# Performance work log

Measured on AMD Instinct MI355X. Metric: run time of the kernel, lower is better.

The kernel has to match this reference:

```python
import jax, jax.numpy as jnp
import numpy as np

RNN_NUM = 4  # rnn_num mean-field iterations


def setup_inputs() -> dict:
    key = jax.random.key(0)
    k1, k2, k3, k4 = jax.random.split(key, 4)
    T, N, M, K = 16384, 256, 8, 16  # time steps, regions, features, gaussian kernels
    inputs = jax.random.normal(k1, (T, N, M), dtype=jnp.float32)
    kernels = jax.random.uniform(k2, (N, N, K), dtype=jnp.float32)  # positive -> stable denominator
    W_feat = jax.random.uniform(k3, (1, M), dtype=jnp.float32) * 0.01  # feature_linear_layer.weight (F_in[1]=1, F_in[0]=M)
    W_lin = jax.random.uniform(k4, (1, K), dtype=jnp.float32) * 0.01   # linear_layer.weight (1, D_in)
    return {"inputs": inputs, "kernels": kernels, "W_feat": W_feat, "W_lin": W_lin}


def reference(inputs, kernels, W_feat, W_lin):
    # inputs: (T, N, M); kernels: (N, N, K); W_feat: (1, M); W_lin: (1, K)
    x = inputs @ W_feat.T                 # feature_layer -> (T, N, 1)
    originals = x
    # feature_layer(ones(T,N,M)) is constant: every entry equals sum(W_feat)
    f_weights = jnp.sum(W_feat)           # scalar, broadcasts as (T, N, 1)
    # static_conv_layer(all_ones, kernels): conv1d with length-1 input of ones
    # == row-sum of each kernel slice -> (N, K); loop-invariant, compute once.
    ones_conv = kernels.sum(axis=1)       # (N, K)
    denom = f_weights + 2.0 * (ones_conv @ W_lin.T)  # (N, 1), broadcasts over T
    for _ in range(RNN_NUM):
        # static_conv_layer(x, kernels): conv1d(length=1) == matmul per kernel slice,
        # fused over all K slices: out[t,i,k] = sum_j x[t,j] * kernels[i,j,k]
        conv = jnp.einsum('tj,ijk->tik', x[:, :, 0], kernels)  # (T, N, K)
        numer = originals + 2.0 * (conv @ W_lin.T)             # (T, N, 1)
        x = numer / denom
    return x
```

## Files before the change

kernel.cpp:

```cpp
#include <hip/hip_runtime.h>


#define NREG 256
#define KG   16
#define MF   8

typedef unsigned short u16;
typedef __attribute__((ext_vector_type(8))) short short8;
typedef __attribute__((ext_vector_type(4))) float f32x4;

__device__ __forceinline__ void async_copy16(const void* g, void* l) {
    __builtin_amdgcn_global_load_lds(
        (const __attribute__((address_space(1))) void*)g,
        (__attribute__((address_space(3))) void*)l,
        16, 0, 0);
}

__device__ __forceinline__ f32x4 ld16(const float* p) {
    f32x4 d;
    asm volatile("global_load_dwordx4 %0, %1, off" : "=v"(d) : "v"(p));
    return d;
}

__device__ __forceinline__ u16 bf16_rne(float x) {
    unsigned u = __float_as_uint(x);
    return (u16)((u + 0x7FFFu + ((u >> 16) & 1u)) >> 16);
}
__device__ __forceinline__ float bf16_to_f(u16 h) {
    return __uint_as_float(((unsigned)h) << 16);
}

__global__ __launch_bounds__(256) void k_prep(const float* __restrict__ kern,
                                              const float* __restrict__ Wlin,
                                              const float* __restrict__ Wfeat,
                                              float* __restrict__ B,
                                              float* __restrict__ Einv) {
    const int i = blockIdx.x, j = threadIdx.x;
    const float* kp = kern + ((size_t)i * NREG + j) * KG;
    float4 w0 = *(const float4*)(Wlin + 0);
    float4 w1 = *(const float4*)(Wlin + 4);
    float4 w2 = *(const float4*)(Wlin + 8);
    float4 w3 = *(const float4*)(Wlin + 12);
    float4 v0 = *(const float4*)(kp + 0);
    float4 v1 = *(const float4*)(kp + 4);
    float4 v2 = *(const float4*)(kp + 8);
    float4 v3 = *(const float4*)(kp + 12);
    float km = v0.x*w0.x + v0.y*w0.y + v0.z*w0.z + v0.w*w0.w
             + v1.x*w1.x + v1.y*w1.y + v1.z*w1.z + v1.w*w1.w
             + v2.x*w2.x + v2.y*w2.y + v2.z*w2.z + v2.w*w2.w
             + v3.x*w3.x + v3.y*w3.y + v3.z*w3.z + v3.w*w3.w;

    __shared__ float red[256];
    red[j] = km;
    __syncthreads();
    for (int s = 128; s > 0; s >>= 1) {
        if (j < s) red[j] += red[j + s];
        __syncthreads();
    }
    __shared__ float sden;
    if (j == 0) {
        float fw = 0.f;
#pragma unroll
        for (int m = 0; m < MF; ++m) fw += Wfeat[m];
        float den = fw + 2.f * red[0];
        sden = den;
        Einv[i] = 1.f / den;
    }
    __syncthreads();
    B[(size_t)i * NREG + j] = 2.f * km / sden;
}

#define MM1_BODY(Ar, Bm, acc)                                                 \
    _Pragma("unroll 4")                                                       \
    for (int l = 0; l < NREG; l += 8) {                                       \
        float b0 = Bm[(size_t)(l + 0) * NREG + tid];                          \
        float b1 = Bm[(size_t)(l + 1) * NREG + tid];                          \
        float b2 = Bm[(size_t)(l + 2) * NREG + tid];                          \
        float b3 = Bm[(size_t)(l + 3) * NREG + tid];                          \
        float b4 = Bm[(size_t)(l + 4) * NREG + tid];                          \
        float b5 = Bm[(size_t)(l + 5) * NREG + tid];                          \
        float b6 = Bm[(size_t)(l + 6) * NREG + tid];                          \
        float b7 = Bm[(size_t)(l + 7) * NREG + tid];                          \
        acc += Ar[l+0]*b0 + Ar[l+1]*b1 + Ar[l+2]*b2 + Ar[l+3]*b3              \
             + Ar[l+4]*b4 + Ar[l+5]*b5 + Ar[l+6]*b6 + Ar[l+7]*b7;             \
    }

__global__ __launch_bounds__(256) void k_mm(const float* __restrict__ A,
                                            const float* __restrict__ Bm,
                                            float* __restrict__ Out) {
    const int tid = threadIdx.x;
    const int i = blockIdx.x;
    __shared__ float Ar[NREG];
    Ar[tid] = A[(size_t)i * NREG + tid];
    __syncthreads();
    float acc = 0.f;
    MM1_BODY(Ar, Bm, acc)
    Out[(size_t)i * NREG + tid] = acc;
}

__global__ __launch_bounds__(256) void k_mm2comb(const float* __restrict__ B,
                                                 const float* __restrict__ C,
                                                 const float* __restrict__ Einv,
                                                 u16* __restrict__ Mh,
                                                 u16* __restrict__ Ml) {
    const int tid = threadIdx.x;
    const int i = blockIdx.x;
    __shared__ float Ar[NREG];

    Ar[tid] = B[(size_t)i * NREG + tid];
    __syncthreads();
    float g1 = 0.f;
    MM1_BODY(Ar, C, g1)
    __syncthreads();
    Ar[tid] = C[(size_t)i * NREG + tid];
    __syncthreads();
    float g2 = 0.f;
    MM1_BODY(Ar, C, g2)

    const size_t idx = (size_t)i * NREG + tid;
    float v = ((i == tid) ? 1.f : 0.f) + B[idx] + C[idx] + g1;
    v = v * Einv[tid] + g2;
    u16 h = bf16_rne(v);
    Mh[idx] = h;
    Ml[idx] = bf16_rne(v - bf16_to_f(h));
}

__global__ __launch_bounds__(512, 1) void k_main(const float* __restrict__ in,
                                                 const float* __restrict__ Wfeat,
                                                 const u16* __restrict__ Mh,
                                                 const u16* __restrict__ Ml,
                                                 float* __restrict__ out) {
    __shared__ __align__(16) u16 Ah[64 * 256];
    __shared__ __align__(16) u16 Al[64 * 256];
    __shared__ __align__(16) u16 Bh[256 * 64];
    __shared__ __align__(16) u16 Bl[256 * 64];

    const int tid = threadIdx.x, lane = tid & 63, wid = tid >> 6;
    const size_t t0 = (size_t)blockIdx.x * 64;

    float4 wa = *(const float4*)(Wfeat);
    float4 wb = *(const float4*)(Wfeat + 4);
    asm volatile("" :: "v"(wa.x), "v"(wa.y), "v"(wa.z), "v"(wa.w),
                       "v"(wb.x), "v"(wb.y), "v"(wb.z), "v"(wb.w));

    const float* rowbase = in + (t0 + wid * 8) * (NREG * MF);

#define ISSUE(BUF, TL)                                                        \
    {                                                                         \
        const float* rp_ = rowbase + (TL) * 2048 + lane * 8;                  \
        _Pragma("unroll")                                                     \
        for (int q = 0; q < 8; ++q)                                           \
            BUF[q] = ld16(rp_ + (q >> 1) * 512 + (q & 1) * 4);                \
    }

#define PROCESS(BUF, TL)                                                      \
    {                                                                         \
        const int t_ = wid * 8 + (TL);                                        \
        _Pragma("unroll")                                                     \
        for (int dq = 0; dq < 4; ++dq) {                                      \
            f32x4 a0 = BUF[2 * dq], a1 = BUF[2 * dq + 1];                     \
            float o = a0[0]*wa.x + a0[1]*wa.y + a0[2]*wa.z + a0[3]*wa.w       \
                    + a1[0]*wb.x + a1[1]*wb.y + a1[2]*wb.z + a1[3]*wb.w;      \
            u16 h_ = bf16_rne(o);                                             \
            u16 l_ = bf16_rne(o - bf16_to_f(h_));                             \
            const int j_ = dq * 64 + lane;                                    \
            const int idx_ = t_ * 256 + (((j_ >> 3) ^ (TL)) * 8) + (j_ & 7);  \
            Ah[idx_] = h_;                                                    \
            Al[idx_] = l_;                                                    \
        }                                                                     \
    }

#define WAITV(N)  asm volatile("s_waitcnt vmcnt(" #N ")" ::: "memory");       \
                  __builtin_amdgcn_sched_barrier(0);

    f32x4 ba[8], bb[8];
    ISSUE(ba, 0)
    ISSUE(bb, 1)
    WAITV(8)  PROCESS(ba, 0)  ISSUE(ba, 2)
    WAITV(8)  PROCESS(bb, 1)  ISSUE(bb, 3)
    WAITV(8)  PROCESS(ba, 2)  ISSUE(ba, 4)
    WAITV(8)  PROCESS(bb, 3)  ISSUE(bb, 5)
    WAITV(8)  PROCESS(ba, 4)  ISSUE(ba, 6)
    WAITV(8)  PROCESS(bb, 5)  ISSUE(bb, 7)
    WAITV(8)  PROCESS(ba, 6)
    WAITV(0)  PROCESS(bb, 7)

    __syncthreads();

    const int mrow = (wid >> 1) * 16 + (lane & 15);
    const int nh   = (wid & 1) * 8;
    f32x4 acc[8];
#pragma unroll
    for (int n = 0; n < 8; ++n) acc[n] = (f32x4){0.f, 0.f, 0.f, 0.f};

    for (int p = 0; p < 4; ++p) {
        if (p) __syncthreads();
#pragma unroll
        for (int s = 0; s < 8; ++s) {
            const int g = s * 8 + wid;
            const int i0 = (g & 31) * 8;
            const u16* sg = (g >> 5) ? Ml : Mh;
            u16* dg = (g >> 5) ? Bl : Bh;
            const int irow = i0 + (lane >> 3);
            const int ch = (lane & 7) ^ (lane >> 3);
            async_copy16(sg + (size_t)irow * NREG + p * 64 + ch * 8,
                         dg + i0 * 64);
        }
        __syncthreads();

#pragma unroll
        for (int kst = 0; kst < 2; ++kst) {
            const int achunk = (8 * p + 4 * kst + (lane >> 4)) ^ (lane & 7);
            short8 a_h = *(const short8*)(Ah + mrow * 256 + achunk * 8);
            short8 a_l = *(const short8*)(Al + mrow * 256 + achunk * 8);
#pragma unroll
            for (int n = 0; n < 8; ++n) {
                const int irow = (nh + n) * 16 + (lane & 15);
                const int bchunk = (4 * kst + (lane >> 4)) ^ (lane & 7);
                short8 b_h = *(const short8*)(Bh + irow * 64 + bchunk * 8);
                short8 b_l = *(const short8*)(Bl + irow * 64 + bchunk * 8);
                acc[n] = __builtin_amdgcn_mfma_f32_16x16x32_bf16(a_h, b_h, acc[n], 0, 0, 0);
                acc[n] = __builtin_amdgcn_mfma_f32_16x16x32_bf16(a_h, b_l, acc[n], 0, 0, 0);
                acc[n] = __builtin_amdgcn_mfma_f32_16x16x32_bf16(a_l, b_h, acc[n], 0, 0, 0);
            }
        }
    }

    const size_t tbase = t0 + (wid >> 1) * 16 + (lane >> 4) * 4;
#pragma unroll
    for (int n = 0; n < 8; ++n) {
#pragma unroll
        for (int r = 0; r < 4; ++r) {
            out[(tbase + r) * NREG + (nh + n) * 16 + (lane & 15)] = acc[n][r];
        }
    }
}

extern "C" void kernel_launch(void* const* d_in, const int* in_sizes, int n_in,
                              void* d_out, int out_size, void* d_ws, size_t ws_size,
                              hipStream_t stream) {
    const float* inputs  = (const float*)d_in[0];
    const float* kernels = (const float*)d_in[1];
    const float* Wfeat   = (const float*)d_in[2];
    const float* Wlin    = (const float*)d_in[3];
    float* out = (float*)d_out;

    float* ws   = (float*)d_ws;
    float* B    = ws;
    float* C    = B  + NREG * NREG;
    float* Einv = C  + NREG * NREG;
    u16*   Mh   = (u16*)(Einv + NREG);
    u16*   Ml   = Mh + NREG * NREG;

    k_prep    <<<256, 256, 0, stream>>>(kernels, Wlin, Wfeat, B, Einv);
    k_mm      <<<256, 256, 0, stream>>>(B, B, C);
    k_mm2comb <<<256, 256, 0, stream>>>(B, C, Einv, Mh, Ml);
    k_main    <<<256, 512, 0, stream>>>(inputs, Wfeat, Mh, Ml, out);
}
```

Before: 56.34 us.

## Fuse matrix-power precompute into one row-wise kernel with split-K threads

```diff
diff --git a/kernel.cpp b/kernel.cpp
--- a/kernel.cpp
+++ b/kernel.cpp
@@ -70,59 +70,55 @@
     B[(size_t)i * NREG + j] = 2.f * km / sden;
 }
 
-#define MM1_BODY(Ar, Bm, acc)                                                 \
-    _Pragma("unroll 4")                                                       \
-    for (int l = 0; l < NREG; l += 8) {                                       \
-        float b0 = Bm[(size_t)(l + 0) * NREG + tid];                          \
-        float b1 = Bm[(size_t)(l + 1) * NREG + tid];                          \
-        float b2 = Bm[(size_t)(l + 2) * NREG + tid];                          \
-        float b3 = Bm[(size_t)(l + 3) * NREG + tid];                          \
-        float b4 = Bm[(size_t)(l + 4) * NREG + tid];                          \
-        float b5 = Bm[(size_t)(l + 5) * NREG + tid];                          \
-        float b6 = Bm[(size_t)(l + 6) * NREG + tid];                          \
-        float b7 = Bm[(size_t)(l + 7) * NREG + tid];                          \
-        acc += Ar[l+0]*b0 + Ar[l+1]*b1 + Ar[l+2]*b2 + Ar[l+3]*b3              \
-             + Ar[l+4]*b4 + Ar[l+5]*b5 + Ar[l+6]*b6 + Ar[l+7]*b7;             \
-    }
-
-__global__ __launch_bounds__(256) void k_mm(const float* __restrict__ A,
-                                            const float* __restrict__ Bm,
-                                            float* __restrict__ Out) {
-    const int tid = threadIdx.x;
+__global__ __launch_bounds__(512) void k_rows(const float* __restrict__ B,
+                                              const float* __restrict__ Einv,
+                                              u16* __restrict__ Mh,
+                                              u16* __restrict__ Ml) {
     const int i = blockIdx.x;
-    __shared__ float Ar[NREG];
-    Ar[tid] = A[(size_t)i * NREG + tid];
-    __syncthreads();
-    float acc = 0.f;
-    MM1_BODY(Ar, Bm, acc)
-    Out[(size_t)i * NREG + tid] = acc;
-}
-
-__global__ __launch_bounds__(256) void k_mm2comb(const float* __restrict__ B,
-                                                 const float* __restrict__ C,
-                                                 const float* __restrict__ Einv,
-                                                 u16* __restrict__ Mh,
-                                                 u16* __restrict__ Ml) {
-    const int tid = threadIdx.x;
-    const int i = blockIdx.x;
-    __shared__ float Ar[NREG];
-
-    Ar[tid] = B[(size_t)i * NREG + tid];
-    __syncthreads();
-    float g1 = 0.f;
-    MM1_BODY(Ar, C, g1)
-    __syncthreads();
-    Ar[tid] = C[(size_t)i * NREG + tid];
-    __syncthreads();
-    float g2 = 0.f;
-    MM1_BODY(Ar, C, g2)
-
-    const size_t idx = (size_t)i * NREG + tid;
-    float v = ((i == tid) ? 1.f : 0.f) + B[idx] + C[idx] + g1;
-    v = v * Einv[tid] + g2;
-    u16 h = bf16_rne(v);
-    Mh[idx] = h;
-    Ml[idx] = bf16_rne(v - bf16_to_f(h));
+    const int j = threadIdx.x & 255;
+    const int h = threadIdx.x >> 8;
+    const int l0 = h * 128;
+    __shared__ float rB[NREG], rP[NREG];
+    __shared__ float part[2][NREG];
+
+    if (h == 0) rB[j] = B[(size_t)i * NREG + j];
+    __syncthreads();
+
+#define ROWMM(rowv, dst_write)                                                \
+    {                                                                         \
+        float acc = 0.f;                                                      \
+        _Pragma("unroll 4")                                                   \
+        for (int l = l0; l < l0 + 128; l += 8) {                              \
+            float b0 = B[(size_t)(l + 0) * NREG + j];                         \
+            float b1 = B[(size_t)(l + 1) * NREG + j];                         \
+            float b2 = B[(size_t)(l + 2) * NREG + j];                         \
+            float b3 = B[(size_t)(l + 3) * NREG + j];                         \
+            float b4 = B[(size_t)(l + 4) * NREG + j];                         \
+            float b5 = B[(size_t)(l + 5) * NREG + j];                         \
+            float b6 = B[(size_t)(l + 6) * NREG + j];                         \
+            float b7 = B[(size_t)(l + 7) * NREG + j];                         \
+            acc += rowv[l+0]*b0 + rowv[l+1]*b1 + rowv[l+2]*b2 + rowv[l+3]*b3  \
+                 + rowv[l+4]*b4 + rowv[l+5]*b5 + rowv[l+6]*b6 + rowv[l+7]*b7; \
+        }                                                                     \
+        part[h][j] = acc;                                                     \
+        __syncthreads();                                                      \
+        dst_write                                                             \
+        __syncthreads();                                                      \
+    }
+
+    float b2v = 0.f, b3v = 0.f, b4v = 0.f;
+    ROWMM(rB,  { b2v = part[0][j] + part[1][j]; if (h == 0) rP[j] = b2v; })
+    ROWMM(rP,  { b3v = part[0][j] + part[1][j]; if (h == 1) rP[j] = b3v; })
+    ROWMM(rP,  { b4v = part[0][j] + part[1][j]; })
+
+    if (h == 0) {
+        const size_t idx = (size_t)i * NREG + j;
+        float v = ((i == j) ? 1.f : 0.f) + rB[j] + b2v + b3v;
+        v = v * Einv[j] + b4v;
+        u16 hh = bf16_rne(v);
+        Mh[idx] = hh;
+        Ml[idx] = bf16_rne(v - bf16_to_f(hh));
+    }
 }
 
 __global__ __launch_bounds__(512, 1) void k_main(const float* __restrict__ in,
@@ -247,13 +243,11 @@
 
     float* ws   = (float*)d_ws;
     float* B    = ws;
-    float* C    = B  + NREG * NREG;
-    float* Einv = C  + NREG * NREG;
+    float* Einv = B + NREG * NREG;
     u16*   Mh   = (u16*)(Einv + NREG);
     u16*   Ml   = Mh + NREG * NREG;
 
-    k_prep    <<<256, 256, 0, stream>>>(kernels, Wlin, Wfeat, B, Einv);
-    k_mm      <<<256, 256, 0, stream>>>(B, B, C);
-    k_mm2comb <<<256, 256, 0, stream>>>(B, C, Einv, Mh, Ml);
-    k_main    <<<256, 512, 0, stream>>>(inputs, Wfeat, Mh, Ml, out);
-}
+    k_prep <<<256, 256, 0, stream>>>(kernels, Wlin, Wfeat, B, Einv);
+    k_rows <<<256, 512, 0, stream>>>(B, Einv, Mh, Ml);
+    k_main <<<256, 512, 0, stream>>>(inputs, Wfeat, Mh, Ml, out);
+}
```

Result: faster. 50.30 us (-10.7%).
